# Performance work log

Hardware: AMD Instinct MI355X
Metric: run time of the kernel (lower is better)

## Reference

```python
import jax, jax.numpy as jnp
import numpy as np

B, S, D, H = 2, 2048, 512, 8
DH = D // H  # depth per head = 64
MAX_SEQ = 2048


def setup_inputs() -> dict:
    key = jax.random.key(0)
    ks = jax.random.split(key, 12)
    sc = 1.0 / np.sqrt(D)
    inp = {
        "v": jax.random.normal(ks[0], (B, S, D), jnp.float32),
        "k": jax.random.normal(ks[1], (B, S, D), jnp.float32),
        "q": jax.random.normal(ks[2], (B, S, D), jnp.float32),
        # causal look-ahead mask: 1.0 where attention is disallowed (j > i)
        "mask": jnp.triu(jnp.ones((S, S), jnp.float32), k=1)[None, None, :, :],
        "Wq": jax.random.normal(ks[3], (D, D), jnp.float32) * sc,
        "bq": jnp.zeros((D,), jnp.float32),
        "Wk": jax.random.normal(ks[4], (D, D), jnp.float32) * sc,
        "bk": jnp.zeros((D,), jnp.float32),
        "Wv": jax.random.normal(ks[5], (D, D), jnp.float32) * sc,
        "bv": jnp.zeros((D,), jnp.float32),
        "Wo": jax.random.normal(ks[6], (D, D), jnp.float32) * sc,
        "bo": jnp.zeros((D,), jnp.float32),
        # relative position embedding table [max_seq, depth]
        "E": jax.random.normal(ks[7], (MAX_SEQ, DH), jnp.float32) * 0.02,
    }
    return inp


def reference(v, k, q, mask, Wq, bq, Wk, bk, Wv, bv, Wo, bo, E):
    b, s, d = q.shape
    split = lambda x: x.reshape(b, s, H, DH).transpose(0, 2, 1, 3)  # [b,h,s,dh]
    qh = split(q @ Wq + bq)
    kh = split(k @ Wk + bk)
    vh = split(v @ Wv + bv)

    # QK^T logits [b,h,lq,lk]
    logits = jnp.einsum("bhqd,bhkd->bhqk", qh, kh)

    # relative position bias (Music Transformer skewing trick)
    Eq = E[max(MAX_SEQ - s, 0):, :]          # left embedding slice [s, dh]
    m = Eq.shape[0]
    QE = jnp.einsum("bhld,md->bhlm", qh, Eq)  # [b,h,s,m]
    # keep entries where col >= m-1-row (qe masking)
    rows = jnp.arange(s)[:, None]
    cols = jnp.arange(m)[None, :]
    QE = QE * (cols >= (m - 1 - rows)).astype(QE.dtype)
    # skew: pad one zero column on the left, reshape, drop first row
    padded = jnp.pad(QE, ((0, 0), (0, 0), (0, 0), (1, 0)))  # [b,h,s,m+1]
    Srel = padded.reshape(b, H, m + 1, s)[:, :, 1:, :]       # [b,h,m,s]
    # here len_q == len_k == s, so Srel is [b,h,s,s] with no extra pad/slice

    logits = (logits + Srel) / jnp.sqrt(jnp.float32(DH))
    logits = logits + mask * -1e9
    attn = jax.nn.softmax(logits, axis=-1)
    out = jnp.einsum("bhqk,bhkd->bhqd", attn, vh)
    out = out.transpose(0, 2, 1, 3).reshape(b, s, d)
    return out @ Wo + bo, attn
```

## Files before the change

### kernel.cpp

```cpp
#include <hip/hip_runtime.h>

typedef __bf16 bf16x8 __attribute__((ext_vector_type(8)));
typedef float f32x4 __attribute__((ext_vector_type(4)));

#define MFMA(a, b, c) __builtin_amdgcn_mfma_f32_16x16x32_bf16((a), (b), (c), 0, 0, 0)

__global__ __launch_bounds__(256)
void prep_kernel(const float* __restrict__ Wq, const float* __restrict__ Wk,
                 const float* __restrict__ Wv, const float* __restrict__ Wo,
                 const float* __restrict__ E,
                 __bf16* __restrict__ WT, __bf16* __restrict__ Ebf)
{
    __shared__ float tl[32][33];
    const int bx = blockIdx.x, t = threadIdx.x;
    if (bx < 1024) {
        const int wi = bx >> 8, tile = bx & 255;
        const float* W = wi == 0 ? Wq : wi == 1 ? Wk : wi == 2 ? Wv : Wo;
        __bf16* dst = WT + (size_t)wi * 512 * 512;
        const int k0 = (tile >> 4) << 5, n0 = (tile & 15) << 5;
        const int tx = t & 31, ty = t >> 5;
        #pragma unroll
        for (int i = 0; i < 4; ++i) {
            int r = ty + i * 8;
            tl[r][tx] = W[(size_t)(k0 + r) * 512 + n0 + tx];
        }
        __syncthreads();
        #pragma unroll
        for (int i = 0; i < 4; ++i) {
            int r = ty + i * 8;
            dst[(size_t)(n0 + r) * 512 + k0 + tx] = (__bf16)tl[tx][r];
        }
    } else {
        int idx = (bx - 1024) * 256 + t;
        for (int i = idx; i < 2048 * 64; i += 8 * 256)
            Ebf[i] = (__bf16)E[i];
    }
}

__global__ __launch_bounds__(256, 3)
void proj_kernel(const float* __restrict__ xq, const float* __restrict__ xk,
                 const float* __restrict__ xv, const __bf16* __restrict__ WT,
                 const float* __restrict__ bq, const float* __restrict__ bk,
                 const float* __restrict__ bv,
                 __bf16* __restrict__ outQ, __bf16* __restrict__ outK,
                 __bf16* __restrict__ outV)
{
    __shared__ __bf16 As[128][72];
    __shared__ __bf16 Bs[64][72];
    const int t = threadIdx.x;
    const int z = blockIdx.y;
    const float* x = z == 0 ? xq : z == 1 ? xk : xv;
    const float* bias = z == 0 ? bq : z == 1 ? bk : bv;
    const __bf16* Wt = WT + (size_t)z * (512 * 512);
    __bf16* outp = z == 0 ? outQ : z == 1 ? outK : outV;

    const int bx = blockIdx.x;
    const int m0 = (bx >> 3) << 7;
    const int n0 = (bx & 7) << 6;
    const int w = t >> 6, lane = t & 63, quad = lane >> 4, l16 = lane & 15;

    const int ar = t >> 1, ac = (t & 1) << 5;
    const int br = t >> 2, bc = (t & 3) << 4;

    float4 xr[8];
    int4 wr0, wr1;
    {
        const float4* xs = (const float4*)(x + (size_t)(m0 + ar) * 512 + ac);
        #pragma unroll
        for (int j = 0; j < 8; ++j) xr[j] = xs[j];
        const int4* wsrc = (const int4*)(Wt + (size_t)(n0 + br) * 512 + bc);
        wr0 = wsrc[0]; wr1 = wsrc[1];
    }

    f32x4 acc[2][4];
    #pragma unroll
    for (int rb = 0; rb < 2; ++rb)
        #pragma unroll
        for (int nt = 0; nt < 4; ++nt) acc[rb][nt] = (f32x4)0.f;

    for (int k0 = 0; k0 < 512; k0 += 64) {
        __syncthreads();
        {
            __bf16 tb[32];
            #pragma unroll
            for (int j = 0; j < 8; ++j) {
                tb[j * 4 + 0] = (__bf16)xr[j].x;
                tb[j * 4 + 1] = (__bf16)xr[j].y;
                tb[j * 4 + 2] = (__bf16)xr[j].z;
                tb[j * 4 + 3] = (__bf16)xr[j].w;
            }
            *(int4*)&As[ar][ac]      = ((int4*)tb)[0];
            *(int4*)&As[ar][ac + 8]  = ((int4*)tb)[1];
            *(int4*)&As[ar][ac + 16] = ((int4*)tb)[2];
            *(int4*)&As[ar][ac + 24] = ((int4*)tb)[3];
            *(int4*)&Bs[br][bc]     = wr0;
            *(int4*)&Bs[br][bc + 8] = wr1;
        }
        __syncthreads();
        if (k0 + 64 < 512) {
            const float4* xs = (const float4*)(x + (size_t)(m0 + ar) * 512 + k0 + 64 + ac);
            #pragma unroll
            for (int j = 0; j < 8; ++j) xr[j] = xs[j];
            const int4* wsrc = (const int4*)(Wt + (size_t)(n0 + br) * 512 + k0 + 64 + bc);
            wr0 = wsrc[0]; wr1 = wsrc[1];
        }
        bf16x8 bf[8];
        #pragma unroll
        for (int nt = 0; nt < 4; ++nt) {
            bf[nt * 2]     = *(const bf16x8*)&Bs[nt * 16 + l16][quad * 8];
            bf[nt * 2 + 1] = *(const bf16x8*)&Bs[nt * 16 + l16][32 + quad * 8];
        }
        #pragma unroll
        for (int rb = 0; rb < 2; ++rb) {
            bf16x8 a0 = *(const bf16x8*)&As[w * 32 + rb * 16 + l16][quad * 8];
            bf16x8 a1 = *(const bf16x8*)&As[w * 32 + rb * 16 + l16][32 + quad * 8];
            #pragma unroll
            for (int nt = 0; nt < 4; ++nt) {
                acc[rb][nt] = MFMA(a0, bf[nt * 2], acc[rb][nt]);
                acc[rb][nt] = MFMA(a1, bf[nt * 2 + 1], acc[rb][nt]);
            }
        }
    }
    #pragma unroll
    for (int rb = 0; rb < 2; ++rb) {
        #pragma unroll
        for (int nt = 0; nt < 4; ++nt) {
            const int n = n0 + nt * 16 + l16;
            const float bb = bias[n];
            const int h = n >> 6, dh = n & 63;
            #pragma unroll
            for (int i = 0; i < 4; ++i) {
                const int m = m0 + w * 32 + rb * 16 + quad * 4 + i;
                const int b = m >> 11, s = m & 2047;
                outp[(((size_t)(b * 8 + h) * 2048 + s) << 6) + dh] = (__bf16)(acc[rb][nt][i] + bb);
            }
        }
    }
}

__global__ __launch_bounds__(256, 2)
void attn_kernel(const __bf16* __restrict__ Qh, const __bf16* __restrict__ Kh,
                 const __bf16* __restrict__ Vh, const __bf16* __restrict__ Eb,
                 __bf16* __restrict__ Pout, float* __restrict__ Linv,
                 __bf16* __restrict__ ctx)
{
    __shared__ __bf16 Qs[64][72];
    __shared__ __bf16 Ks[64][72];
    __shared__ __bf16 Vs[64][72];
    __shared__ __bf16 Es[128][72];

    const int t = threadIdx.x;
    const int bx = blockIdx.x;
    const int tt = bx & 31;
    const int bh = ((bx & 255) >> 5) + ((bx >> 8) << 3);
    const int q0 = (bx < 256 ? (31 - tt) : tt) << 6;
    const int w = t >> 6, lane = t & 63, quad = lane >> 4, l16 = lane & 15;
    const int qw = w << 4;

    const __bf16* Qg = Qh + (size_t)bh * (2048 * 64);
    const __bf16* Kg = Kh + (size_t)bh * (2048 * 64);
    const __bf16* Vg = Vh + (size_t)bh * (2048 * 64);
    __bf16* Pg = Pout + (size_t)bh * (2048 * 2048);

    {
        int r = t >> 2, c0 = (t & 3) << 4;
        const int4* src = (const int4*)(Qg + (size_t)(q0 + r) * 64 + c0);
        int4 v0 = src[0], v1 = src[1];
        *(int4*)&Qs[r][c0]     = v0;
        *(int4*)&Qs[r][c0 + 8] = v1;
    }
    __syncthreads();
    const bf16x8 qa0 = *(const bf16x8*)&Qs[qw + l16][quad * 8];
    const bf16x8 qa1 = *(const bf16x8*)&Qs[qw + l16][32 + quad * 8];
    __syncthreads();

    __bf16 (* const Ps)[72] = Qs;

    const int kr = t >> 2, kc = (t & 3) << 4;
    const int er = t >> 1, ec = (t & 1) << 5;

    int4 kreg0, kreg1, ereg0, ereg1, ereg2, ereg3, vreg0, vreg1;

    const int nkt = (q0 >> 6) + 1;

    float lsum[4] = {0.f, 0.f, 0.f, 0.f};
    f32x4 acc_o[4];
    #pragma unroll
    for (int i = 0; i < 4; ++i) acc_o[i] = (f32x4)0.f;

    {
        const int4* ks = (const int4*)(Kg + (size_t)kr * 64 + kc);
        kreg0 = ks[0]; kreg1 = ks[1];
        int e = 1984 - q0 + er; if (e > 2047) e = 2047;
        const int4* es = (const int4*)(Eb + (size_t)e * 64 + ec);
        ereg0 = es[0]; ereg1 = es[1]; ereg2 = es[2]; ereg3 = es[3];
        const int4* vs = (const int4*)(Vg + (size_t)kr * 64 + kc);
        vreg0 = vs[0]; vreg1 = vs[1];
    }

    const float csc = 0.125f * 1.44269504f;

    for (int kt = 0; kt < nkt; ++kt) {
        const int k0 = kt << 6;
        __syncthreads();
        *(int4*)&Ks[kr][kc]     = kreg0;
        *(int4*)&Ks[kr][kc + 8] = kreg1;
        *(int4*)&Es[er][ec]      = ereg0;
        *(int4*)&Es[er][ec + 8]  = ereg1;
        *(int4*)&Es[er][ec + 16] = ereg2;
        *(int4*)&Es[er][ec + 24] = ereg3;
        {
            __bf16 tmp[16];
            *(int4*)&tmp[0] = vreg0; *(int4*)&tmp[8] = vreg1;
            #pragma unroll
            for (int j = 0; j < 16; ++j) {
                const int dh = kc + j;
                Vs[dh][kr ^ (((dh >> 4) & 1) << 3)] = tmp[j];
            }
        }
        __syncthreads();

        if (kt + 1 < nkt) {
            const int k0n = (kt + 1) << 6;
            const int4* ks = (const int4*)(Kg + (size_t)(k0n + kr) * 64 + kc);
            kreg0 = ks[0]; kreg1 = ks[1];
            int e = 1984 - q0 + k0n + er; if (e > 2047) e = 2047;
            const int4* es = (const int4*)(Eb + (size_t)e * 64 + ec);
            ereg0 = es[0]; ereg1 = es[1]; ereg2 = es[2]; ereg3 = es[3];
            const int4* vs = (const int4*)(Vg + (size_t)(k0n + kr) * 64 + kc);
            vreg0 = vs[0]; vreg1 = vs[1];
        }

        f32x4 aqk[4];
        #pragma unroll
        for (int nt = 0; nt < 4; ++nt) {
            aqk[nt] = (f32x4)0.f;
            bf16x8 b0 = *(const bf16x8*)&Ks[nt * 16 + l16][quad * 8];
            bf16x8 b1 = *(const bf16x8*)&Ks[nt * 16 + l16][32 + quad * 8];
            aqk[nt] = MFMA(qa0, b0, aqk[nt]);
            aqk[nt] = MFMA(qa1, b1, aqk[nt]);
        }
        f32x4 aqe[5];
        #pragma unroll
        for (int jj = 0; jj < 5; ++jj) {
            aqe[jj] = (f32x4)0.f;
            const int ebr = 48 - qw + jj * 16 + l16;
            bf16x8 b0 = *(const bf16x8*)&Es[ebr][quad * 8];
            bf16x8 b1 = *(const bf16x8*)&Es[ebr][32 + quad * 8];
            aqe[jj] = MFMA(qa0, b0, aqe[jj]);
            aqe[jj] = MFMA(qa1, b1, aqe[jj]);
        }

        #pragma unroll
        for (int i = 0; i < 4; ++i) {
            const int d  = quad * 4 + i;
            const int ql = qw + d;
            const int qq = q0 + ql;
            const int sp = (l16 + 15 - d) & 15;
            const bool hi = l16 > d;
            #pragma unroll
            for (int nt = 0; nt < 4; ++nt) {
                float g0 = __shfl(aqe[nt][i], sp, 16);
                float g1 = __shfl(aqe[nt + 1][i], sp, 16);
                float qe = hi ? g1 : g0;
                float ev = (k0 + nt * 16 + l16 <= qq)
                         ? exp2f((aqk[nt][i] + qe) * csc) : 0.f;
                lsum[i] += ev;
                __bf16 pb = (__bf16)ev;
                Pg[(size_t)qq * 2048 + k0 + nt * 16 + l16] = pb;
                Ps[ql][nt * 16 + l16] = pb;
            }
        }

        const bf16x8 pa0 = *(const bf16x8*)&Ps[qw + l16][quad * 8];
        const bf16x8 pa1 = *(const bf16x8*)&Ps[qw + l16][32 + quad * 8];
        #pragma unroll
        for (int dt = 0; dt < 4; ++dt) {
            const int xr = (dt & 1) << 3;
            bf16x8 vb0 = *(const bf16x8*)&Vs[dt * 16 + l16][(quad * 8) ^ xr];
            bf16x8 vb1 = *(const bf16x8*)&Vs[dt * 16 + l16][32 + ((quad * 8) ^ xr)];
            acc_o[dt] = MFMA(pa0, vb0, acc_o[dt]);
            acc_o[dt] = MFMA(pa1, vb1, acc_o[dt]);
        }
    }

    float linv[4];
    #pragma unroll
    for (int i = 0; i < 4; ++i) {
        float v = lsum[i];
        #pragma unroll
        for (int m = 1; m < 16; m <<= 1) v += __shfl_xor(v, m, 16);
        linv[i] = 1.0f / v;
    }

    {
        const int b = bh >> 3, h = bh & 7;
        #pragma unroll
        for (int dt = 0; dt < 4; ++dt) {
            #pragma unroll
            for (int i = 0; i < 4; ++i) {
                const int qq = q0 + qw + quad * 4 + i;
                const int d = dt * 16 + l16;
                ctx[((size_t)(b * 2048 + qq) * 512) + h * 64 + d] =
                    (__bf16)(acc_o[dt][i] * linv[i]);
            }
        }
    }
    if (l16 == 0) {
        #pragma unroll
        for (int i = 0; i < 4; ++i)
            Linv[(size_t)bh * 2048 + q0 + qw + quad * 4 + i] = linv[i];
    }
}

__global__ __launch_bounds__(256)
void norm_kernel(const __bf16* __restrict__ Pin, const float* __restrict__ Linv,
                 float* __restrict__ attn)
{
    const int blk = blockIdx.x;
    const int bh = blk >> 9;
    const int r0 = (blk & 511) << 2;
    const int t = threadIdx.x;
    const int q = r0 + (t >> 6);
    const int c0 = (t & 63) << 5;
    const float li = Linv[(size_t)bh * 2048 + q];
    const int qend = ((q >> 6) + 1) << 6;
    const __bf16* prow = Pin + ((size_t)bh * 2048 + q) * 2048;
    float* arow = attn + ((size_t)bh * 2048 + q) * 2048;

    if (c0 < qend) {
        #pragma unroll
        for (int j = 0; j < 4; ++j) {
            int4 raw = *(const int4*)(prow + c0 + j * 8);
            bf16x8 pv = *(bf16x8*)&raw;
            float4 o0, o1;
            o0.x = (float)pv[0] * li; o0.y = (float)pv[1] * li;
            o0.z = (float)pv[2] * li; o0.w = (float)pv[3] * li;
            o1.x = (float)pv[4] * li; o1.y = (float)pv[5] * li;
            o1.z = (float)pv[6] * li; o1.w = (float)pv[7] * li;
            *(float4*)(arow + c0 + j * 8)     = o0;
            *(float4*)(arow + c0 + j * 8 + 4) = o1;
        }
    } else {
        const float4 z4 = make_float4(0.f, 0.f, 0.f, 0.f);
        #pragma unroll
        for (int j = 0; j < 8; ++j)
            *(float4*)(arow + c0 + j * 4) = z4;
    }
}

__global__ __launch_bounds__(256, 2)
void outproj_kernel(const __bf16* __restrict__ ctx, const __bf16* __restrict__ WoT,
                    const float* __restrict__ bo, float* __restrict__ out)
{
    __shared__ __bf16 As[64][72];
    __shared__ __bf16 Bs[64][72];
    const int t = threadIdx.x;
    const int bx = blockIdx.x;
    const int m0 = (bx >> 3) << 6;
    const int n0 = (bx & 7) << 6;
    const int w = t >> 6, lane = t & 63, quad = lane >> 4, l16 = lane & 15;
    const int r = t >> 2, c0 = (t & 3) << 4;

    int4 ar0, ar1, br0, br1;
    {
        const int4* asrc = (const int4*)(ctx + (size_t)(m0 + r) * 512 + c0);
        ar0 = asrc[0]; ar1 = asrc[1];
        const int4* bsrc = (const int4*)(WoT + (size_t)(n0 + r) * 512 + c0);
        br0 = bsrc[0]; br1 = bsrc[1];
    }

    f32x4 acc[4];
    #pragma unroll
    for (int i = 0; i < 4; ++i) acc[i] = (f32x4)0.f;

    for (int k0 = 0; k0 < 512; k0 += 64) {
        __syncthreads();
        *(int4*)&As[r][c0]     = ar0;
        *(int4*)&As[r][c0 + 8] = ar1;
        *(int4*)&Bs[r][c0]     = br0;
        *(int4*)&Bs[r][c0 + 8] = br1;
        __syncthreads();
        if (k0 + 64 < 512) {
            const int4* asrc = (const int4*)(ctx + (size_t)(m0 + r) * 512 + k0 + 64 + c0);
            ar0 = asrc[0]; ar1 = asrc[1];
            const int4* bsrc = (const int4*)(WoT + (size_t)(n0 + r) * 512 + k0 + 64 + c0);
            br0 = bsrc[0]; br1 = bsrc[1];
        }
        bf16x8 a0 = *(const bf16x8*)&As[(w << 4) + l16][quad * 8];
        bf16x8 a1 = *(const bf16x8*)&As[(w << 4) + l16][32 + quad * 8];
        #pragma unroll
        for (int nt = 0; nt < 4; ++nt) {
            bf16x8 b0 = *(const bf16x8*)&Bs[nt * 16 + l16][quad * 8];
            bf16x8 b1 = *(const bf16x8*)&Bs[nt * 16 + l16][32 + quad * 8];
            acc[nt] = MFMA(a0, b0, acc[nt]);
            acc[nt] = MFMA(a1, b1, acc[nt]);
        }
    }
    #pragma unroll
    for (int nt = 0; nt < 4; ++nt) {
        const int n = n0 + nt * 16 + l16;
        const float bb = bo[n];
        #pragma unroll
        for (int i = 0; i < 4; ++i) {
            const int m = m0 + (w << 4) + quad * 4 + i;
            out[(size_t)m * 512 + n] = acc[nt][i] + bb;
        }
    }
}

extern "C" void kernel_launch(void* const* d_in, const int* in_sizes, int n_in,
                              void* d_out, int out_size, void* d_ws, size_t ws_size,
                              hipStream_t stream) {
    const float* v  = (const float*)d_in[0];
    const float* k  = (const float*)d_in[1];
    const float* q  = (const float*)d_in[2];
    const float* Wq = (const float*)d_in[4];
    const float* bq = (const float*)d_in[5];
    const float* Wk = (const float*)d_in[6];
    const float* bk = (const float*)d_in[7];
    const float* Wv = (const float*)d_in[8];
    const float* bv = (const float*)d_in[9];
    const float* Wo = (const float*)d_in[10];
    const float* bo = (const float*)d_in[11];
    const float* E  = (const float*)d_in[12];

    float* out  = (float*)d_out;
    float* attn = out + (size_t)2 * 2048 * 512;

    char* ws = (char*)d_ws;
    __bf16* WT   = (__bf16*)ws;
    __bf16* Ebf  = (__bf16*)(ws + (size_t)(4 * 512 * 512) * 2);
    __bf16* Qh   = Ebf + (size_t)2048 * 64;
    __bf16* Kh   = Qh + (size_t)16 * 2048 * 64;
    __bf16* Vh   = Kh + (size_t)16 * 2048 * 64;
    __bf16* ctx  = Vh + (size_t)16 * 2048 * 64;
    __bf16* Pout = ctx + (size_t)16 * 2048 * 64;
    float*  Linv = (float*)(Pout + (size_t)16 * 2048 * 2048);

    prep_kernel<<<1032, 256, 0, stream>>>(Wq, Wk, Wv, Wo, E, WT, Ebf);
    proj_kernel<<<dim3(256, 3), 256, 0, stream>>>(q, k, v, WT, bq, bk, bv, Qh, Kh, Vh);
    attn_kernel<<<512, 256, 0, stream>>>(Qh, Kh, Vh, Ebf, Pout, Linv, ctx);
    norm_kernel<<<8192, 256, 0, stream>>>(Pout, Linv, attn);
    outproj_kernel<<<512, 256, 0, stream>>>(ctx, WT + (size_t)3 * 512 * 512, bo, out);
}
```

Measured before the change: 495.5 us.

## Fuse softmax normalization into attention via two-pass P then PV with attn write

The attention kernel is split into two passes. The first computes unnormalized probabilities and row sums, staging each P tile through shared memory and writing it to global memory with coalesced vector stores. The second re-reads P, multiplies by V, and writes the normalized fp32 attention matrix plus the zero upper triangle directly, so the separate norm kernel and its Linv buffer go away. Occupancy is also raised to 3 blocks per SM by dropping one LDS buffer, at the cost of reading P back from global memory (likely from cache) and loading V in a separate loop.

```diff
diff --git a/kernel.cpp b/kernel.cpp
--- a/kernel.cpp
+++ b/kernel.cpp
@@ -138,16 +138,16 @@
     }
 }
 
-__global__ __launch_bounds__(256, 2)
+__global__ __launch_bounds__(256, 3)
 void attn_kernel(const __bf16* __restrict__ Qh, const __bf16* __restrict__ Kh,
                  const __bf16* __restrict__ Vh, const __bf16* __restrict__ Eb,
-                 __bf16* __restrict__ Pout, float* __restrict__ Linv,
+                 __bf16* __restrict__ Pout, float* __restrict__ attn,
                  __bf16* __restrict__ ctx)
 {
-    __shared__ __bf16 Qs[64][72];
-    __shared__ __bf16 Ks[64][72];
-    __shared__ __bf16 Vs[64][72];
-    __shared__ __bf16 Es[128][72];
+    __shared__ __bf16 SA[64][72];
+    __shared__ __bf16 SB[64][72];
+    __shared__ __bf16 SC[128][72];
+    __shared__ float linv_s[64];
 
     const int t = threadIdx.x;
     const int bx = blockIdx.x;
@@ -161,82 +161,70 @@
     const __bf16* Kg = Kh + (size_t)bh * (2048 * 64);
     const __bf16* Vg = Vh + (size_t)bh * (2048 * 64);
     __bf16* Pg = Pout + (size_t)bh * (2048 * 2048);
-
-    {
-        int r = t >> 2, c0 = (t & 3) << 4;
-        const int4* src = (const int4*)(Qg + (size_t)(q0 + r) * 64 + c0);
+    float* attng = attn + (size_t)bh * (2048 * 2048);
+
+    const int sr = t >> 2, sc = (t & 3) << 4;
+    const int er = t >> 1, ec = (t & 1) << 5;
+
+    {
+        const int4* src = (const int4*)(Qg + (size_t)(q0 + sr) * 64 + sc);
         int4 v0 = src[0], v1 = src[1];
-        *(int4*)&Qs[r][c0]     = v0;
-        *(int4*)&Qs[r][c0 + 8] = v1;
+        *(int4*)&SA[sr][sc]     = v0;
+        *(int4*)&SA[sr][sc + 8] = v1;
     }
     __syncthreads();
-    const bf16x8 qa0 = *(const bf16x8*)&Qs[qw + l16][quad * 8];
-    const bf16x8 qa1 = *(const bf16x8*)&Qs[qw + l16][32 + quad * 8];
+    const bf16x8 qa0 = *(const bf16x8*)&SA[qw + l16][quad * 8];
+    const bf16x8 qa1 = *(const bf16x8*)&SA[qw + l16][32 + quad * 8];
     __syncthreads();
 
-    __bf16 (* const Ps)[72] = Qs;
-
-    const int kr = t >> 2, kc = (t & 3) << 4;
-    const int er = t >> 1, ec = (t & 1) << 5;
-
-    int4 kreg0, kreg1, ereg0, ereg1, ereg2, ereg3, vreg0, vreg1;
+    __bf16 (* const Ps)[72] = SA;
 
     const int nkt = (q0 >> 6) + 1;
+    const float csc = 0.125f * 1.44269504f;
 
     float lsum[4] = {0.f, 0.f, 0.f, 0.f};
-    f32x4 acc_o[4];
-    #pragma unroll
-    for (int i = 0; i < 4; ++i) acc_o[i] = (f32x4)0.f;
-
-    {
-        const int4* ks = (const int4*)(Kg + (size_t)kr * 64 + kc);
+
+    int4 kreg0, kreg1, ereg0, ereg1, ereg2, ereg3;
+    {
+        const int4* ks = (const int4*)(Kg + (size_t)sr * 64 + sc);
         kreg0 = ks[0]; kreg1 = ks[1];
         int e = 1984 - q0 + er; if (e > 2047) e = 2047;
         const int4* es = (const int4*)(Eb + (size_t)e * 64 + ec);
         ereg0 = es[0]; ereg1 = es[1]; ereg2 = es[2]; ereg3 = es[3];
-        const int4* vs = (const int4*)(Vg + (size_t)kr * 64 + kc);
-        vreg0 = vs[0]; vreg1 = vs[1];
-    }
-
-    const float csc = 0.125f * 1.44269504f;
+    }
 
     for (int kt = 0; kt < nkt; ++kt) {
         const int k0 = kt << 6;
-        __syncthreads();
-        *(int4*)&Ks[kr][kc]     = kreg0;
-        *(int4*)&Ks[kr][kc + 8] = kreg1;
-        *(int4*)&Es[er][ec]      = ereg0;
-        *(int4*)&Es[er][ec + 8]  = ereg1;
-        *(int4*)&Es[er][ec + 16] = ereg2;
-        *(int4*)&Es[er][ec + 24] = ereg3;
-        {
-            __bf16 tmp[16];
-            *(int4*)&tmp[0] = vreg0; *(int4*)&tmp[8] = vreg1;
-            #pragma unroll
-            for (int j = 0; j < 16; ++j) {
-                const int dh = kc + j;
-                Vs[dh][kr ^ (((dh >> 4) & 1) << 3)] = tmp[j];
-            }
-        }
+        if (kt > 0) {
+            int4 p0 = *(const int4*)&Ps[sr][sc];
+            int4 p1 = *(const int4*)&Ps[sr][sc + 8];
+            __bf16* dst = Pg + (size_t)(q0 + sr) * 2048 + (k0 - 64) + sc;
+            *(int4*)dst       = p0;
+            *(int4*)(dst + 8) = p1;
+        }
+        *(int4*)&SB[sr][sc]     = kreg0;
+        *(int4*)&SB[sr][sc + 8] = kreg1;
+        *(int4*)&SC[er][ec]      = ereg0;
+        *(int4*)&SC[er][ec + 8]  = ereg1;
+        *(int4*)&SC[er][ec + 16] = ereg2;
+        *(int4*)&SC[er][ec + 24] = ereg3;
         __syncthreads();
 
         if (kt + 1 < nkt) {
             const int k0n = (kt + 1) << 6;
-            const int4* ks = (const int4*)(Kg + (size_t)(k0n + kr) * 64 + kc);
+            const int4* ks = (const int4*)(Kg + (size_t)(k0n + sr) * 64 + sc);
             kreg0 = ks[0]; kreg1 = ks[1];
             int e = 1984 - q0 + k0n + er; if (e > 2047) e = 2047;
             const int4* es = (const int4*)(Eb + (size_t)e * 64 + ec);
             ereg0 = es[0]; ereg1 = es[1]; ereg2 = es[2]; ereg3 = es[3];
-            const int4* vs = (const int4*)(Vg + (size_t)(k0n + kr) * 64 + kc);
-            vreg0 = vs[0]; vreg1 = vs[1];
         }
 
         f32x4 aqk[4];
         #pragma unroll
         for (int nt = 0; nt < 4; ++nt) {
             aqk[nt] = (f32x4)0.f;
-            bf16x8 b0 = *(const bf16x8*)&Ks[nt * 16 + l16][quad * 8];
-            bf16x8 b1 = *(const bf16x8*)&Ks[nt * 16 + l16][32 + quad * 8];
+            bf16x8 b0 = *(const bf16x8*)&SB[nt * 16 + l16][quad * 8];
+            bf16x8 b1 = *(const bf16x8*)&SB[nt * 16 + l16][32 + quad * 8];
             aqk[nt] = MFMA(qa0, b0, aqk[nt]);
             aqk[nt] = MFMA(qa1, b1, aqk[nt]);
         }
@@ -245,8 +233,8 @@
         for (int jj = 0; jj < 5; ++jj) {
             aqe[jj] = (f32x4)0.f;
             const int ebr = 48 - qw + jj * 16 + l16;
-            bf16x8 b0 = *(const bf16x8*)&Es[ebr][quad * 8];
-            bf16x8 b1 = *(const bf16x8*)&Es[ebr][32 + quad * 8];
+            bf16x8 b0 = *(const bf16x8*)&SC[ebr][quad * 8];
+            bf16x8 b1 = *(const bf16x8*)&SC[ebr][32 + quad * 8];
             aqe[jj] = MFMA(qa0, b0, aqe[jj]);
             aqe[jj] = MFMA(qa1, b1, aqe[jj]);
         }
@@ -266,31 +254,93 @@
                 float ev = (k0 + nt * 16 + l16 <= qq)
                          ? exp2f((aqk[nt][i] + qe) * csc) : 0.f;
                 lsum[i] += ev;
-                __bf16 pb = (__bf16)ev;
-                Pg[(size_t)qq * 2048 + k0 + nt * 16 + l16] = pb;
-                Ps[ql][nt * 16 + l16] = pb;
-            }
-        }
-
-        const bf16x8 pa0 = *(const bf16x8*)&Ps[qw + l16][quad * 8];
-        const bf16x8 pa1 = *(const bf16x8*)&Ps[qw + l16][32 + quad * 8];
+                Ps[ql][nt * 16 + l16] = (__bf16)ev;
+            }
+        }
+        __syncthreads();
+    }
+    {
+        int4 p0 = *(const int4*)&Ps[sr][sc];
+        int4 p1 = *(const int4*)&Ps[sr][sc + 8];
+        __bf16* dst = Pg + (size_t)(q0 + sr) * 2048 + ((nkt - 1) << 6) + sc;
+        *(int4*)dst       = p0;
+        *(int4*)(dst + 8) = p1;
+    }
+    {
+        #pragma unroll
+        for (int i = 0; i < 4; ++i) {
+            float v = lsum[i];
+            #pragma unroll
+            for (int m = 1; m < 16; m <<= 1) v += __shfl_xor(v, m, 16);
+            if (l16 == 0) linv_s[qw + quad * 4 + i] = 1.0f / v;
+        }
+    }
+    __syncthreads();
+
+    const float li = linv_s[qw + l16];
+    float linvr[4];
+    #pragma unroll
+    for (int i = 0; i < 4; ++i) linvr[i] = linv_s[qw + quad * 4 + i];
+
+    f32x4 acc_o[4];
+    #pragma unroll
+    for (int i = 0; i < 4; ++i) acc_o[i] = (f32x4)0.f;
+
+    int4 vreg0, vreg1;
+    {
+        const int4* vs = (const int4*)(Vg + (size_t)sr * 64 + sc);
+        vreg0 = vs[0]; vreg1 = vs[1];
+    }
+
+    for (int kt = 0; kt < nkt; ++kt) {
+        const int k0 = kt << 6;
+        __syncthreads();
+        {
+            __bf16 tmp[16];
+            *(int4*)&tmp[0] = vreg0; *(int4*)&tmp[8] = vreg1;
+            #pragma unroll
+            for (int j = 0; j < 16; ++j) {
+                const int dh = sc + j;
+                SB[dh][sr ^ (((dh >> 4) & 1) << 3)] = tmp[j];
+            }
+        }
+        __syncthreads();
+        if (kt + 1 < nkt) {
+            const int4* vs = (const int4*)(Vg + (size_t)(((kt + 1) << 6) + sr) * 64 + sc);
+            vreg0 = vs[0]; vreg1 = vs[1];
+        }
+
+        const __bf16* prow = Pg + (size_t)(q0 + qw + l16) * 2048 + k0 + quad * 8;
+        int4 praw0 = *(const int4*)prow;
+        int4 praw1 = *(const int4*)(prow + 32);
+        bf16x8 pa0 = *(bf16x8*)&praw0;
+        bf16x8 pa1 = *(bf16x8*)&praw1;
+
         #pragma unroll
         for (int dt = 0; dt < 4; ++dt) {
             const int xr = (dt & 1) << 3;
-            bf16x8 vb0 = *(const bf16x8*)&Vs[dt * 16 + l16][(quad * 8) ^ xr];
-            bf16x8 vb1 = *(const bf16x8*)&Vs[dt * 16 + l16][32 + ((quad * 8) ^ xr)];
+            bf16x8 vb0 = *(const bf16x8*)&SB[dt * 16 + l16][(quad * 8) ^ xr];
+            bf16x8 vb1 = *(const bf16x8*)&SB[dt * 16 + l16][32 + ((quad * 8) ^ xr)];
             acc_o[dt] = MFMA(pa0, vb0, acc_o[dt]);
             acc_o[dt] = MFMA(pa1, vb1, acc_o[dt]);
         }
-    }
-
-    float linv[4];
-    #pragma unroll
-    for (int i = 0; i < 4; ++i) {
-        float v = lsum[i];
-        #pragma unroll
-        for (int m = 1; m < 16; m <<= 1) v += __shfl_xor(v, m, 16);
-        linv[i] = 1.0f / v;
+
+        {
+            float* arow = attng + (size_t)(q0 + qw + l16) * 2048 + k0 + quad * 8;
+            float4 o;
+            o.x = (float)pa0[0] * li; o.y = (float)pa0[1] * li;
+            o.z = (float)pa0[2] * li; o.w = (float)pa0[3] * li;
+            *(float4*)arow = o;
+            o.x = (float)pa0[4] * li; o.y = (float)pa0[5] * li;
+            o.z = (float)pa0[6] * li; o.w = (float)pa0[7] * li;
+            *(float4*)(arow + 4) = o;
+            o.x = (float)pa1[0] * li; o.y = (float)pa1[1] * li;
+            o.z = (float)pa1[2] * li; o.w = (float)pa1[3] * li;
+            *(float4*)(arow + 32) = o;
+            o.x = (float)pa1[4] * li; o.y = (float)pa1[5] * li;
+            o.z = (float)pa1[6] * li; o.w = (float)pa1[7] * li;
+            *(float4*)(arow + 36) = o;
+        }
     }
 
     {
@@ -302,50 +352,21 @@
                 const int qq = q0 + qw + quad * 4 + i;
                 const int d = dt * 16 + l16;
                 ctx[((size_t)(b * 2048 + qq) * 512) + h * 64 + d] =
-                    (__bf16)(acc_o[dt][i] * linv[i]);
-            }
-        }
-    }
-    if (l16 == 0) {
-        #pragma unroll
-        for (int i = 0; i < 4; ++i)
-            Linv[(size_t)bh * 2048 + q0 + qw + quad * 4 + i] = linv[i];
-    }
-}
-
-__global__ __launch_bounds__(256)
-void norm_kernel(const __bf16* __restrict__ Pin, const float* __restrict__ Linv,
-                 float* __restrict__ attn)
-{
-    const int blk = blockIdx.x;
-    const int bh = blk >> 9;
-    const int r0 = (blk & 511) << 2;
-    const int t = threadIdx.x;
-    const int q = r0 + (t >> 6);
-    const int c0 = (t & 63) << 5;
-    const float li = Linv[(size_t)bh * 2048 + q];
-    const int qend = ((q >> 6) + 1) << 6;
-    const __bf16* prow = Pin + ((size_t)bh * 2048 + q) * 2048;
-    float* arow = attn + ((size_t)bh * 2048 + q) * 2048;
-
-    if (c0 < qend) {
-        #pragma unroll
-        for (int j = 0; j < 4; ++j) {
-            int4 raw = *(const int4*)(prow + c0 + j * 8);
-            bf16x8 pv = *(bf16x8*)&raw;
-            float4 o0, o1;
-            o0.x = (float)pv[0] * li; o0.y = (float)pv[1] * li;
-            o0.z = (float)pv[2] * li; o0.w = (float)pv[3] * li;
-            o1.x = (float)pv[4] * li; o1.y = (float)pv[5] * li;
-            o1.z = (float)pv[6] * li; o1.w = (float)pv[7] * li;
-            *(float4*)(arow + c0 + j * 8)     = o0;
-            *(float4*)(arow + c0 + j * 8 + 4) = o1;
-        }
-    } else {
-        const float4 z4 = make_float4(0.f, 0.f, 0.f, 0.f);
-        #pragma unroll
-        for (int j = 0; j < 8; ++j)
-            *(float4*)(arow + c0 + j * 4) = z4;
+                    (__bf16)(acc_o[dt][i] * linvr[i]);
+            }
+        }
+    }
+    {
+        const int kend = q0 + 64;
+        const int zc = 2048 - kend;
+        if (zc > 0) {
+            const int zq = zc >> 2;
+            const float4 z4 = make_float4(0.f, 0.f, 0.f, 0.f);
+            for (int idx = t; idx < 64 * zq; idx += 256) {
+                int r = idx / zq, c = idx - r * zq;
+                *(float4*)&attng[(size_t)(q0 + r) * 2048 + kend + c * 4] = z4;
+            }
+        }
     }
 }
 
@@ -436,11 +457,9 @@
     __bf16* Vh   = Kh + (size_t)16 * 2048 * 64;
     __bf16* ctx  = Vh + (size_t)16 * 2048 * 64;
     __bf16* Pout = ctx + (size_t)16 * 2048 * 64;
-    float*  Linv = (float*)(Pout + (size_t)16 * 2048 * 2048);
 
     prep_kernel<<<1032, 256, 0, stream>>>(Wq, Wk, Wv, Wo, E, WT, Ebf);
     proj_kernel<<<dim3(256, 3), 256, 0, stream>>>(q, k, v, WT, bq, bk, bv, Qh, Kh, Vh);
-    attn_kernel<<<512, 256, 0, stream>>>(Qh, Kh, Vh, Ebf, Pout, Linv, ctx);
-    norm_kernel<<<8192, 256, 0, stream>>>(Pout, Linv, attn);
+    attn_kernel<<<512, 256, 0, stream>>>(Qh, Kh, Vh, Ebf, Pout, attn, ctx);
     outproj_kernel<<<512, 256, 0, stream>>>(ctx, WT + (size_t)3 * 512 * 512, bo, out);
 }
```

After: 454.8 us. -8.2%, faster.
